# Optimization experiments

Measured on AMD Instinct MI355X. Metric: run time of the kernel, lower is better.

Reference implementation:

```python
import jax, jax.numpy as jnp
import numpy as np

N = 100000   # nodes
E = 1600000  # edges
D = 64       # in/hidden channels


def setup_inputs() -> dict:
    key = jax.random.key(0)
    ks = jax.random.split(key, 8)
    x = jax.random.normal(ks[0], (N, D), dtype=jnp.float32)
    edge_index = jax.random.randint(ks[1], (2, E), 0, N, dtype=jnp.int32)
    s = 1.0 / np.sqrt(D)
    W1 = jax.random.uniform(ks[2], (D, D), jnp.float32, -s, s)
    W2 = jax.random.uniform(ks[3], (D, D), jnp.float32, -s, s)
    W3 = jax.random.uniform(ks[4], (D, D), jnp.float32, -s, s)
    b1 = jnp.zeros((D,), jnp.float32)
    b2 = jnp.zeros((D,), jnp.float32)
    b3 = jnp.zeros((D,), jnp.float32)
    return {"x": x, "edge_index": edge_index,
            "W1": W1, "b1": b1, "W2": W2, "b2": b2, "W3": W3, "b3": b3}


def _gcn_conv(x, src, dst, deg_inv_sqrt, W, b):
    # norm = d^{-1/2}[src] * d^{-1/2}[dst] (symmetric GCN normalization w/ self-loops)
    norm = deg_inv_sqrt[src] * deg_inv_sqrt[dst]        # [E+N]
    h = x @ W                                           # [N, D] dense GEMM
    msg = h[src] * norm[:, None]                        # gather + scale
    out = jax.ops.segment_sum(msg, dst, num_segments=x.shape[0])  # scatter-add
    return out + b


def reference(x, edge_index, W1, b1, W2, b2, W3, b3):
    n = x.shape[0]
    loop = jnp.arange(n, dtype=edge_index.dtype)
    src = jnp.concatenate([edge_index[0], loop])        # add self-loops
    dst = jnp.concatenate([edge_index[1], loop])
    deg = jax.ops.segment_sum(jnp.ones_like(src, x.dtype), dst, num_segments=n)
    deg_inv_sqrt = jnp.where(deg > 0, jax.lax.rsqrt(jnp.maximum(deg, 1.0)), 0.0)

    h = _gcn_conv(x, src, dst, deg_inv_sqrt, W1, b1)
    h = jax.nn.relu(h)                                  # dropout is identity (eval)
    h = _gcn_conv(h, src, dst, deg_inv_sqrt, W2, b2)
    h = jax.nn.relu(h)
    out = _gcn_conv(h, src, dst, deg_inv_sqrt, W3, b3)
    return out
```

## Files before the change

### kernel.cpp

```cpp
#include <hip/hip_runtime.h>
#include <hip/hip_fp16.h>
#include <type_traits>

#define DCH 64
#define NBSHIFT 7
#define BROWS 128
#define MAXNB 1024
#define CAPB 2816
#define CAP 4096
#define CHUNK 2048

__global__ __launch_bounds__(256) void bucket_scatter(const int* __restrict__ src,
        const int* __restrict__ dst, int* __restrict__ cursor,
        unsigned int* __restrict__ tmp, int E, int NB) {
    __shared__ int hist[MAXNB];
    __shared__ int res[MAXNB];
    const int base_e = blockIdx.x * CHUNK;
    const int nloc = min(CHUNK, E - base_e);
    for (int i = threadIdx.x; i < NB; i += blockDim.x) hist[i] = 0;
    __syncthreads();
    for (int i = threadIdx.x; i < nloc; i += blockDim.x)
        atomicAdd(&hist[dst[base_e + i] >> NBSHIFT], 1);
    __syncthreads();
    for (int i = threadIdx.x; i < NB; i += blockDim.x) {
        int c = hist[i];
        res[i] = c ? (i * CAPB + atomicAdd(&cursor[i], c)) : 0;
        hist[i] = 0;
    }
    __syncthreads();
    for (int i = threadIdx.x; i < nloc; i += blockDim.x) {
        int d = dst[base_e + i];
        int b = d >> NBSHIFT;
        int r = atomicAdd(&hist[b], 1);
        unsigned int packed = ((unsigned int)(d & (BROWS - 1)) << 24) |
                              (unsigned int)src[base_e + i];
        tmp[res[b] + r] = packed;
    }
}

__global__ __launch_bounds__(BROWS) void bucket_to_csr(
        const unsigned int* __restrict__ tmp, const int* __restrict__ cursor,
        int2* __restrict__ range, int* __restrict__ srcs,
        float* __restrict__ dinv, int N) {
    __shared__ int hist[BROWS];
    __shared__ int off[BROWS];
    __shared__ int cur[BROWS];
    __shared__ int stage[CAP];
    const int b = blockIdx.x;
    const int base = b * CAPB;
    const int count = cursor[b];
    const int t = threadIdx.x;
    hist[t] = 0;
    __syncthreads();
    for (int i = t; i < count; i += BROWS)
        atomicAdd(&hist[tmp[base + i] >> 24], 1);
    __syncthreads();
    int v = hist[t];
    off[t] = v;
    __syncthreads();
    for (int o = 1; o < BROWS; o <<= 1) {
        int add = (t >= o) ? off[t - o] : 0;
        __syncthreads();
        off[t] += add;
        __syncthreads();
    }
    int excl = off[t] - v;
    cur[t] = excl;
    int node = (b << NBSHIFT) + t;
    if (node < N) {
        range[node] = make_int2(base + excl, base + excl + v);
        dinv[node]  = rsqrtf((float)v + 1.0f);
    }
    __syncthreads();
    const bool st = (count <= CAP);
    for (int i = t; i < count; i += BROWS) {
        unsigned int p = tmp[base + i];
        int low = p >> 24;
        int s = (int)(p & 0xFFFFFFu);
        int pos = atomicAdd(&cur[low], 1);
        if (st) stage[pos] = s;
        else    srcs[base + pos] = s;
    }
    __syncthreads();
    if (st)
        for (int i = t; i < count; i += BROWS) srcs[base + i] = stage[i];
}

template<typename InT>
__global__ __launch_bounds__(256, 4) void gemm64(const InT* __restrict__ A,
        const float* __restrict__ W, const float* __restrict__ dinv,
        __half* __restrict__ H, int nrows) {
    __shared__ float Wl[64 * 64];
    __shared__ float Al[64 * 68];
    #pragma unroll
    for (int j = 0; j < 4; ++j) {
        int idx = (int)threadIdx.x + j * 256;
        float4 w = ((const float4*)W)[idx];
        *(float4*)&Wl[(idx >> 4) * 64 + (idx & 15) * 4] = w;
    }
    const int tx = threadIdx.x & 15;
    const int ty = threadIdx.x >> 4;
    const int c0 = tx * 4, r0 = ty * 4;
    const int ntiles = (nrows + 63) >> 6;
    for (int tile = blockIdx.x; tile < ntiles; tile += gridDim.x) {
        const int rowbase = tile << 6;
        const int rmax = min(64, nrows - rowbase);
        __syncthreads();
        #pragma unroll
        for (int j = 0; j < 4; ++j) {
            int idx = (int)threadIdx.x + j * 256;
            int r = idx >> 4, kq = idx & 15;
            float4 a;
            if (r < rmax) {
                if constexpr (std::is_same<InT, float>::value) {
                    a = *(const float4*)(A + (size_t)(rowbase + r) * 64 + kq * 4);
                } else {
                    unsigned long long u = *(const unsigned long long*)
                        ((const __half*)A + (size_t)(rowbase + r) * 64 + kq * 4);
                    union { unsigned long long u; __half2 h[2]; } cv; cv.u = u;
                    float2 f0 = __half22float2(cv.h[0]);
                    float2 f1 = __half22float2(cv.h[1]);
                    a = make_float4(f0.x, f0.y, f1.x, f1.y);
                }
            } else a = make_float4(0.f, 0.f, 0.f, 0.f);
            *(float4*)&Al[r * 68 + kq * 4] = a;
        }
        __syncthreads();
        float acc[4][4] = {};
        #pragma unroll 8
        for (int k = 0; k < 64; ++k) {
            float4 wv = *(const float4*)&Wl[k * 64 + c0];
            float a0 = Al[(r0 + 0) * 68 + k];
            float a1 = Al[(r0 + 1) * 68 + k];
            float a2 = Al[(r0 + 2) * 68 + k];
            float a3 = Al[(r0 + 3) * 68 + k];
            acc[0][0] += a0 * wv.x; acc[0][1] += a0 * wv.y; acc[0][2] += a0 * wv.z; acc[0][3] += a0 * wv.w;
            acc[1][0] += a1 * wv.x; acc[1][1] += a1 * wv.y; acc[1][2] += a1 * wv.z; acc[1][3] += a1 * wv.w;
            acc[2][0] += a2 * wv.x; acc[2][1] += a2 * wv.y; acc[2][2] += a2 * wv.z; acc[2][3] += a2 * wv.w;
            acc[3][0] += a3 * wv.x; acc[3][1] += a3 * wv.y; acc[3][2] += a3 * wv.z; acc[3][3] += a3 * wv.w;
        }
        #pragma unroll
        for (int i = 0; i < 4; ++i) {
            int r = r0 + i;
            if (r < rmax) {
                float s = dinv[rowbase + r];
                __half2* ph = (__half2*)(H + (size_t)(rowbase + r) * 64 + c0);
                ph[0] = __floats2half2_rn(acc[i][0] * s, acc[i][1] * s);
                ph[1] = __floats2half2_rn(acc[i][2] * s, acc[i][3] * s);
            }
        }
    }
}

__device__ __forceinline__ void accumh(__half2 acc[4], float4 v) {
    const __half2* hp = (const __half2*)&v;
    #pragma unroll
    for (int j = 0; j < 4; ++j) acc[j] = __hadd2(acc[j], hp[j]);
}

__device__ __forceinline__ float4 row16(const __half* __restrict__ hs, int s, int q) {
    return *(const float4*)((const char*)hs + ((size_t)s << 7) + (q << 4));
}

template<typename OutT>
__global__ __launch_bounds__(256) void aggregate(
    const __half* __restrict__ hs, const int2* __restrict__ range,
    const int* __restrict__ srcs, const float* __restrict__ dinv,
    const float* __restrict__ b, OutT* __restrict__ out, int n, int do_relu)
{
    int wid  = (blockIdx.x * blockDim.x + threadIdx.x) >> 6;
    int lane = threadIdx.x & 63;
    if (wid >= n) return;
    const int g = lane >> 3;
    const int q = lane & 7;
    const int2 be = range[wid];
    const int beg = be.x, end = be.y;
    __half2 zero = __float2half2_rn(0.f);
    __half2 acch[4]  = {zero, zero, zero, zero};
    __half2 acch2[4] = {zero, zero, zero, zero};
    if (g == 7) accumh(acch, row16(hs, wid, q));
    int e = beg + g;
    for (; e + 8 < end; e += 16) {
        int s0 = srcs[e];
        int s1 = srcs[e + 8];
        float4 v0 = row16(hs, s0, q);
        float4 v1 = row16(hs, s1, q);
        accumh(acch, v0);
        accumh(acch2, v1);
    }
    if (e < end) accumh(acch, row16(hs, srcs[e], q));
    float acc[8];
    #pragma unroll
    for (int j = 0; j < 4; ++j) {
        float2 f0 = __half22float2(acch[j]);
        float2 f1 = __half22float2(acch2[j]);
        acc[2 * j]     = f0.x + f1.x;
        acc[2 * j + 1] = f0.y + f1.y;
    }
    #pragma unroll
    for (int j = 0; j < 8; ++j) {
        float a = acc[j];
        a += __shfl_xor(a, 8);
        a += __shfl_xor(a, 16);
        a += __shfl_xor(a, 32);
        acc[j] = a;
    }
    if (g == 0) {
        float dd = dinv[wid];
        float o[8];
        #pragma unroll
        for (int j = 0; j < 8; ++j) {
            float v = acc[j] * dd + b[q * 8 + j];
            o[j] = do_relu ? fmaxf(v, 0.f) : v;
        }
        if constexpr (std::is_same<OutT, __half>::value) {
            union { uint4 u; __half2 h[4]; } cv;
            cv.h[0] = __floats2half2_rn(o[0], o[1]);
            cv.h[1] = __floats2half2_rn(o[2], o[3]);
            cv.h[2] = __floats2half2_rn(o[4], o[5]);
            cv.h[3] = __floats2half2_rn(o[6], o[7]);
            *(uint4*)((__half*)out + (size_t)wid * DCH + q * 8) = cv.u;
        } else {
            float4* po = (float4*)((float*)out + (size_t)wid * DCH + q * 8);
            po[0] = make_float4(o[0], o[1], o[2], o[3]);
            po[1] = make_float4(o[4], o[5], o[6], o[7]);
        }
    }
}

extern "C" void kernel_launch(void* const* d_in, const int* in_sizes, int n_in,
                              void* d_out, int out_size, void* d_ws, size_t ws_size,
                              hipStream_t stream) {
    const float* x  = (const float*)d_in[0];
    const int*   ei = (const int*)d_in[1];
    const float* W1 = (const float*)d_in[2];
    const float* b1 = (const float*)d_in[3];
    const float* W2 = (const float*)d_in[4];
    const float* b2 = (const float*)d_in[5];
    const float* W3 = (const float*)d_in[6];
    const float* b3 = (const float*)d_in[7];

    const int N = in_sizes[0] / DCH;
    const int E = in_sizes[1] / 2;
    const int* src = ei;
    const int* dst = ei + E;
    const int NB = (N + BROWS - 1) >> NBSHIFT;

    char* ws = (char*)d_ws;
    size_t off = 0;
    auto alloc = [&](size_t bytes) { void* p = ws + off; off = (off + bytes + 255) & ~(size_t)255; return p; };
    int*    cursor = (int*)   alloc((size_t)MAXNB * 4);
    int2*   range  = (int2*)  alloc((size_t)N * 8);
    int*    srcs   = (int*)   alloc((size_t)NB * CAPB * 4);
    float*  dinv   = (float*) alloc((size_t)N * 4);
    __half* hs     = (__half*)alloc((size_t)N * DCH * 2);
    __half* agg    = (__half*)alloc((size_t)N * DCH * 2);
    unsigned int* tmp = (unsigned int*)hs;
    float* out = (float*)d_out;

    const int T = 256;
    const int gAG  = (N * DCH + T - 1) / T;
    const int gGM  = (N + 63) / 64;
    const int nchk = (E + CHUNK - 1) / CHUNK;

    hipMemsetAsync(cursor, 0, (size_t)NB * 4, stream);
    bucket_scatter<<<nchk, T, 0, stream>>>(src, dst, cursor, tmp, E, NB);
    bucket_to_csr<<<NB, BROWS, 0, stream>>>(tmp, cursor, range, srcs, dinv, N);

    gemm64<float><<<gGM, T, 0, stream>>>(x, W1, dinv, hs, N);
    aggregate<__half><<<gAG, T, 0, stream>>>(hs, range, srcs, dinv, b1, agg, N, 1);

    gemm64<__half><<<gGM, T, 0, stream>>>(agg, W2, dinv, hs, N);
    aggregate<__half><<<gAG, T, 0, stream>>>(hs, range, srcs, dinv, b2, agg, N, 1);

    gemm64<__half><<<gGM, T, 0, stream>>>(agg, W3, dinv, hs, N);
    aggregate<float><<<gAG, T, 0, stream>>>(hs, range, srcs, dinv, b3, out, N, 0);
}
```

Measured before the change: 246.4 us.

## Stage bucket scatter in shared memory for coalesced writes, use larger buckets

The bucket scatter now does a single pass over the edges. It keeps each edge's packed value and bucket in registers, runs a block-wide prefix scan over the bucket counts, and stages the edges sorted by bucket in shared memory. Global writes then go out contiguously per bucket instead of as scattered stores. Bucket width doubles to 256 rows, chunk size to 4096 and block size to 512, so there are fewer buckets and bucket_to_csr uses larger blocks. This adds shared-memory use and a log-step scan with many barriers, and bucket_to_csr now has to handle more rows per block.

```diff
diff --git a/kernel.cpp b/kernel.cpp
--- a/kernel.cpp
+++ b/kernel.cpp
@@ -3,38 +3,68 @@
 #include <type_traits>
 
 #define DCH 64
-#define NBSHIFT 7
-#define BROWS 128
-#define MAXNB 1024
-#define CAPB 2816
-#define CAP 4096
-#define CHUNK 2048
-
-__global__ __launch_bounds__(256) void bucket_scatter(const int* __restrict__ src,
+#define NBSHIFT 8
+#define BROWS 256
+#define MAXNB 512
+#define CAPB 5120
+#define CAP 8192
+#define CHUNK 4096
+#define SCT 512
+
+__global__ __launch_bounds__(SCT) void bucket_scatter(const int* __restrict__ src,
         const int* __restrict__ dst, int* __restrict__ cursor,
         unsigned int* __restrict__ tmp, int E, int NB) {
     __shared__ int hist[MAXNB];
+    __shared__ int loff[MAXNB];
     __shared__ int res[MAXNB];
+    __shared__ unsigned int stage[CHUNK];
+    __shared__ unsigned short stgb[CHUNK];
     const int base_e = blockIdx.x * CHUNK;
     const int nloc = min(CHUNK, E - base_e);
-    for (int i = threadIdx.x; i < NB; i += blockDim.x) hist[i] = 0;
-    __syncthreads();
-    for (int i = threadIdx.x; i < nloc; i += blockDim.x)
-        atomicAdd(&hist[dst[base_e + i] >> NBSHIFT], 1);
-    __syncthreads();
-    for (int i = threadIdx.x; i < NB; i += blockDim.x) {
-        int c = hist[i];
-        res[i] = c ? (i * CAPB + atomicAdd(&cursor[i], c)) : 0;
-        hist[i] = 0;
-    }
-    __syncthreads();
-    for (int i = threadIdx.x; i < nloc; i += blockDim.x) {
-        int d = dst[base_e + i];
-        int b = d >> NBSHIFT;
-        int r = atomicAdd(&hist[b], 1);
-        unsigned int packed = ((unsigned int)(d & (BROWS - 1)) << 24) |
-                              (unsigned int)src[base_e + i];
-        tmp[res[b] + r] = packed;
+    const int t = threadIdx.x;
+    if (t < NB) hist[t] = 0;
+    __syncthreads();
+    unsigned int pk[CHUNK / SCT];
+    int bk[CHUNK / SCT], rk[CHUNK / SCT];
+    #pragma unroll
+    for (int c = 0; c < CHUNK / SCT; ++c) {
+        int i = t + c * SCT;
+        if (i < nloc) {
+            int d = dst[base_e + i];
+            int b = d >> NBSHIFT;
+            rk[c] = atomicAdd(&hist[b], 1);
+            bk[c] = b;
+            pk[c] = ((unsigned int)(d & (BROWS - 1)) << 24) |
+                    (unsigned int)src[base_e + i];
+        }
+    }
+    __syncthreads();
+    int v = (t < NB) ? hist[t] : 0;
+    loff[t] = v;
+    __syncthreads();
+    for (int o = 1; o < MAXNB; o <<= 1) {
+        int add = (t >= o) ? loff[t - o] : 0;
+        __syncthreads();
+        loff[t] += add;
+        __syncthreads();
+    }
+    int excl = loff[t] - v;
+    loff[t] = excl;
+    if (t < NB) res[t] = v ? (t * CAPB + atomicAdd(&cursor[t], v)) : 0;
+    __syncthreads();
+    #pragma unroll
+    for (int c = 0; c < CHUNK / SCT; ++c) {
+        int i = t + c * SCT;
+        if (i < nloc) {
+            int p = loff[bk[c]] + rk[c];
+            stage[p] = pk[c];
+            stgb[p]  = (unsigned short)bk[c];
+        }
+    }
+    __syncthreads();
+    for (int i = t; i < nloc; i += SCT) {
+        int b = stgb[i];
+        tmp[res[b] + (i - loff[b])] = stage[i];
     }
 }
 
@@ -264,7 +294,7 @@
     const int nchk = (E + CHUNK - 1) / CHUNK;
 
     hipMemsetAsync(cursor, 0, (size_t)NB * 4, stream);
-    bucket_scatter<<<nchk, T, 0, stream>>>(src, dst, cursor, tmp, E, NB);
+    bucket_scatter<<<nchk, SCT, 0, stream>>>(src, dst, cursor, tmp, E, NB);
     bucket_to_csr<<<NB, BROWS, 0, stream>>>(tmp, cursor, range, srcs, dinv, N);
 
     gemm64<float><<<gGM, T, 0, stream>>>(x, W1, dinv, hs, N);
```

New measurement: 223.6 us. 1.1x faster.
